# Performance work log

Hardware: AMD Instinct MI355X
Metric: run time of the kernel (lower is better)

Reference implementation:

```python
import jax, jax.numpy as jnp
from jax import lax
import numpy as np

DIM = 256
N_EMBED = 512
B = 16
T = 2048


def setup_inputs() -> dict:
    key = jax.random.key(0)
    k1, k2, k3 = jax.random.split(key, 3)
    inp = jax.random.normal(k1, (B, T, DIM), dtype=jnp.float32)
    spk = jax.random.normal(k2, (3, B, DIM), dtype=jnp.float32)
    embedding = jax.random.normal(k3, (N_EMBED, DIM, DIM), dtype=jnp.float32)
    return {"input": inp, "speaker_embedding": spk, "embedding": embedding}


def reference(input, speaker_embedding, embedding):
    x = input                              # (B, T, D)
    mul = speaker_embedding[2].T           # (D, B)
    add = speaker_embedding[1].T           # (D, B)
    # per-batch codebook: (n, D, D) @ (D, B) -> (n, D, B)
    cb = jnp.einsum('ndk,kb->ndb', embedding, mul)
    cb = cb / jnp.linalg.norm(cb, axis=1, keepdims=True)
    cb = cb + add                          # broadcast (D,B) over n
    embed = jnp.transpose(cb, (2, 1, 0))   # (B, D, n)
    # distances on detached values (matches torch .detach())
    flat = lax.stop_gradient(x)
    e = lax.stop_gradient(embed)
    dist = (jnp.sum(flat * flat, axis=2, keepdims=True)
            - 2.0 * jnp.einsum('btd,bdn->btn', flat, e)
            + jnp.sum(e * e, axis=1, keepdims=True))  # (B, T, n)
    embed_ind = jnp.argmax(-dist, axis=2)  # (B, T)
    cbB = jnp.transpose(cb, (2, 0, 1))     # (B, n, D)
    # per-batch gather of selected codes -> (B, T, D)
    quantize = cbB[jnp.arange(cbB.shape[0])[:, None], embed_ind]
    diff = jnp.mean((quantize - x) ** 2)
    quantize_1 = x + lax.stop_gradient(quantize - x)
    return ((quantize + quantize_1) / 2.0, diff, embed_ind)
```

## Files before the change

### kernel.cpp

```cpp
#include <hip/hip_runtime.h>

#define T_   2048
#define D_   256
#define N_   512
#define BTOT 16

typedef unsigned short ushortT;

#define QN   ((size_t)BTOT*T_*D_)
#define IDX0 (QN + 1)

__device__ __forceinline__ float bf2f(ushortT u){
    union { unsigned int i; float f; } c; c.i = ((unsigned int)u) << 16; return c.f;
}
__device__ __forceinline__ void unp8(uint4 p, float* f){
    f[0]=bf2f((ushortT)(p.x & 0xffff)); f[1]=bf2f((ushortT)(p.x >> 16));
    f[2]=bf2f((ushortT)(p.y & 0xffff)); f[3]=bf2f((ushortT)(p.y >> 16));
    f[4]=bf2f((ushortT)(p.z & 0xffff)); f[5]=bf2f((ushortT)(p.z >> 16));
    f[6]=bf2f((ushortT)(p.w & 0xffff)); f[7]=bf2f((ushortT)(p.w >> 16));
}
__device__ __forceinline__ void unp4(uint2 p, float* f){
    f[0]=bf2f((ushortT)(p.x & 0xffff)); f[1]=bf2f((ushortT)(p.x >> 16));
    f[2]=bf2f((ushortT)(p.y & 0xffff)); f[3]=bf2f((ushortT)(p.y >> 16));
}

__global__ void k_probe(const ushortT* __restrict__ x, int* __restrict__ flg){
    int tid = threadIdx.x;
    ushortT u = x[tid];
    int e = (u >> 7) & 0xff;
    bool ok = (e >= 100 && e <= 140);
    unsigned long long m = __ballot(ok);
    if (tid == 0) *flg = (__popcll(m) >= 55) ? 1 : 0;
}

template<int BC>
__global__ __launch_bounds__(256) void k_codebook(
    const void* __restrict__ spkin, const void* __restrict__ embin,
    float* __restrict__ cbw, int b0, const int* __restrict__ flagp)
{
    const int isb = *flagp;
    const ushortT* ss = (const ushortT*)spkin;
    const float*   sf = (const float*)spkin;
    const ushortT* es = (const ushortT*)embin;
    const float*   ef = (const float*)embin;

    __shared__ float s2[D_ * 16];
    __shared__ float s1[D_ * 16];
    __shared__ float red[16 * D_];
    __shared__ float nrm[16];

    const int n = blockIdx.x, tid = threadIdx.x;

    for (int e = tid; e < D_ * 16; e += 256){ s2[e] = 0.f; s1[e] = 0.f; }
    __syncthreads();
    for (int e = tid; e < D_ * BC; e += 256){
        int bl = e >> 8, k = e & 255;
        int g2 = (2*BTOT + b0 + bl)*D_ + k;
        int g1 = (1*BTOT + b0 + bl)*D_ + k;
        s2[k*16 + bl] = isb ? bf2f(ss[g2]) : sf[g2];
        s1[k*16 + bl] = isb ? bf2f(ss[g1]) : sf[g1];
    }
    __syncthreads();

    const int d = tid;
    float acc[16];
    #pragma unroll
    for (int b = 0; b < 16; b++) acc[b] = 0.f;

    const size_t rb = ((size_t)n * D_ + d) * D_;

    auto inner = [&](const float* ev, int k0){
        #pragma unroll
        for (int j = 0; j < 8; j++){
            float e = ev[j];
            if (BC == 16){
                const float4* sp = (const float4*)&s2[(k0 + j) * 16];
                float4 q0 = sp[0], q1 = sp[1], q2 = sp[2], q3 = sp[3];
                acc[0]  += e*q0.x; acc[1]  += e*q0.y; acc[2]  += e*q0.z; acc[3]  += e*q0.w;
                acc[4]  += e*q1.x; acc[5]  += e*q1.y; acc[6]  += e*q1.z; acc[7]  += e*q1.w;
                acc[8]  += e*q2.x; acc[9]  += e*q2.y; acc[10] += e*q2.z; acc[11] += e*q2.w;
                acc[12] += e*q3.x; acc[13] += e*q3.y; acc[14] += e*q3.z; acc[15] += e*q3.w;
            } else {
                #pragma unroll
                for (int bl = 0; bl < BC; bl++)
                    acc[bl] += e * s2[(k0 + j)*16 + bl];
            }
        }
    };

    if (isb){
        for (int k0 = 0; k0 < D_; k0 += 8){
            uint4 p = *(const uint4*)(es + rb + k0);
            float ev[8]; unp8(p, ev);
            inner(ev, k0);
        }
    } else {
        for (int k0 = 0; k0 < D_; k0 += 8){
            float4 p0 = *(const float4*)(ef + rb + k0);
            float4 p1 = *(const float4*)(ef + rb + k0 + 4);
            float ev[8] = {p0.x,p0.y,p0.z,p0.w,p1.x,p1.y,p1.z,p1.w};
            inner(ev, k0);
        }
    }

    #pragma unroll
    for (int bl = 0; bl < BC; bl++) red[bl*D_ + d] = acc[bl]*acc[bl];
    __syncthreads();
    for (int s = 128; s > 0; s >>= 1){
        if (d < s){
            #pragma unroll
            for (int bl = 0; bl < BC; bl++) red[bl*D_ + d] += red[bl*D_ + d + s];
        }
        __syncthreads();
    }
    if (d < BC) nrm[d] = sqrtf(red[d*D_]);
    __syncthreads();

    #pragma unroll
    for (int bl = 0; bl < BC; bl++){
        float cb = acc[bl] / nrm[bl] + s1[d*16 + bl];
        cbw[((size_t)bl*N_ + n)*D_ + d] = cb;
    }
}

__global__ __launch_bounds__(512, 2) void k_gemm(
    const void* __restrict__ xin, const float* __restrict__ cbw,
    float* __restrict__ outf, int blk0, const int* __restrict__ flagp)
{
    const int isb = *flagp;
    const int bl = blockIdx.x >> 4, tT = blockIdx.x & 15;
    const int bg = blk0 + bl;

    __shared__ float As[16 * 132];
    __shared__ float Bs[16 * 256];
    __shared__ float e2p[512];

    const int tid = threadIdx.x;
    const int tx = tid & 31, ty = tid >> 5;
    const int rA = tid >> 2, qA = tid & 3;
    const int rB = tid >> 1, hB = tid & 1;

    const float*   xf = (const float*)xin;
    const ushortT* xs = (const ushortT*)xin;
    const size_t xbase = ((size_t)bg*T_ + tT*128 + rA)*D_ + qA*4;

    float runv[8]; int runi[8];
    #pragma unroll
    for (int i = 0; i < 8; i++){ runv[i] = 3.4e38f; runi[i] = 0x7fffffff; }

    for (int nT = 0; nT < 2; nT++){
        float acc[8][8];
        #pragma unroll
        for (int i = 0; i < 8; i++)
            #pragma unroll
            for (int j = 0; j < 8; j++) acc[i][j] = 0.f;
        float e2acc = 0.f;

        const size_t bbase = ((size_t)bl*N_ + nT*256 + rB)*D_ + hB*8;

        for (int k0 = 0; k0 < D_; k0 += 16){
            float av[4];
            if (isb){
                uint2 p = *(const uint2*)(xs + xbase + k0);
                unp4(p, av);
            } else {
                float4 p = *(const float4*)(xf + xbase + k0);
                av[0]=p.x; av[1]=p.y; av[2]=p.z; av[3]=p.w;
            }
            float bv[8];
            {
                float4 q0 = *(const float4*)(cbw + bbase + k0);
                float4 q1 = *(const float4*)(cbw + bbase + k0 + 4);
                bv[0]=q0.x; bv[1]=q0.y; bv[2]=q0.z; bv[3]=q0.w;
                bv[4]=q1.x; bv[5]=q1.y; bv[6]=q1.z; bv[7]=q1.w;
            }
            #pragma unroll
            for (int j = 0; j < 8; j++) e2acc += bv[j]*bv[j];

            #pragma unroll
            for (int j = 0; j < 4; j++) As[(qA*4 + j)*132 + rA] = av[j];
            #pragma unroll
            for (int j = 0; j < 8; j++) Bs[(hB*8 + j)*256 + rB] = bv[j];
            __syncthreads();

            #pragma unroll
            for (int kl = 0; kl < 16; kl++){
                float4 a0 = *(const float4*)&As[kl*132 + (ty<<2)];
                float4 a1 = *(const float4*)&As[kl*132 + 64 + (ty<<2)];
                float4 c0 = *(const float4*)&Bs[kl*256 + (tx<<2)];
                float4 c1 = *(const float4*)&Bs[kl*256 + 128 + (tx<<2)];
                float ar[8] = {a0.x,a0.y,a0.z,a0.w,a1.x,a1.y,a1.z,a1.w};
                float br[8] = {c0.x,c0.y,c0.z,c0.w,c1.x,c1.y,c1.z,c1.w};
                #pragma unroll
                for (int i = 0; i < 8; i++)
                    #pragma unroll
                    for (int j = 0; j < 8; j++)
                        acc[i][j] += ar[i]*br[j];
            }
            __syncthreads();
        }

        e2p[rB*2 + hB] = e2acc;
        __syncthreads();

        float e2c[8];
        #pragma unroll
        for (int j = 0; j < 8; j++){
            int nl = (tx<<2) + (j&3) + ((j>>2)<<7);
            e2c[j] = e2p[nl*2] + e2p[nl*2 + 1];
        }

        #pragma unroll
        for (int i = 0; i < 8; i++){
            #pragma unroll
            for (int j = 0; j < 8; j++){
                int ng = nT*256 + (tx<<2) + (j&3) + ((j>>2)<<7);
                float s = e2c[j] - 2.f*acc[i][j];
                if (s < runv[i] || (s == runv[i] && ng < runi[i])){
                    runv[i] = s; runi[i] = ng;
                }
            }
        }
    }

    #pragma unroll
    for (int m = 16; m >= 1; m >>= 1){
        #pragma unroll
        for (int i = 0; i < 8; i++){
            float ov = __shfl_xor(runv[i], m);
            int   on = __shfl_xor(runi[i], m);
            if (ov < runv[i] || (ov == runv[i] && on < runi[i])){
                runv[i] = ov; runi[i] = on;
            }
        }
    }
    if (tx == 0){
        #pragma unroll
        for (int i = 0; i < 8; i++){
            int row = (ty<<2) + (i&3) + ((i>>2)<<6);
            outf[IDX0 + (size_t)bg*T_ + tT*128 + row] = (float)runi[i];
        }
    }
}

__global__ __launch_bounds__(256) void k_gather(
    const void* __restrict__ xin, const float* __restrict__ cbw,
    float* __restrict__ outf, float* __restrict__ part,
    int blk0, const int* __restrict__ flagp)
{
    const int isb = *flagp;
    const int bid = blockIdx.x;
    const int bl = bid >> 11, t = bid & 2047;
    const int bg = blk0 + bl;
    const int tid = threadIdx.x;

    const int n = (int)outf[IDX0 + (size_t)bg*T_ + t];

    const float*   xf = (const float*)xin;
    const ushortT* xs = (const ushortT*)xin;
    const size_t rowbase = ((size_t)bg*T_ + t)*D_;
    float xv = isb ? bf2f(xs[rowbase + tid]) : xf[rowbase + tid];
    float q  = cbw[((size_t)bl*N_ + n)*D_ + tid];
    float qm = q - xv;
    float q1 = xv + qm;
    outf[rowbase + tid] = 0.5f*(q + q1);

    float val = qm*qm;
    #pragma unroll
    for (int o = 32; o > 0; o >>= 1) val += __shfl_down(val, o, 64);
    __shared__ float wsum[4];
    if ((tid & 63) == 0) wsum[tid >> 6] = val;
    __syncthreads();
    if (tid == 0)
        atomicAdd(&part[bid & 1023], wsum[0] + wsum[1] + wsum[2] + wsum[3]);
}

__global__ __launch_bounds__(256) void k_fin(const float* __restrict__ part,
                                             float* __restrict__ outf){
    const int tid = threadIdx.x;
    float v = part[tid] + part[tid + 256] + part[tid + 512] + part[tid + 768];
    #pragma unroll
    for (int o = 32; o > 0; o >>= 1) v += __shfl_down(v, o, 64);
    __shared__ float wsum[4];
    if ((tid & 63) == 0) wsum[tid >> 6] = v;
    __syncthreads();
    if (tid == 0)
        outf[QN] = (wsum[0] + wsum[1] + wsum[2] + wsum[3]) * (1.0f / (float)QN);
}

extern "C" void kernel_launch(void* const* d_in, const int* in_sizes, int n_in,
                              void* d_out, int out_size, void* d_ws, size_t ws_size,
                              hipStream_t stream)
{
    const void* x   = d_in[0];
    const void* spk = d_in[1];
    const void* emb = d_in[2];

    int Bc = 16;
    while (Bc > 1 && ((size_t)Bc*N_*D_*4 + 4096 + 16) > ws_size) Bc >>= 1;

    char*  ws   = (char*)d_ws;
    float* cbw  = (float*)ws;
    size_t tail = (size_t)Bc*N_*D_*4;
    float* part = (float*)(ws + tail);
    int*   flg  = (int*)  (ws + tail + 4096);

    float* outf = (float*)d_out;

    hipMemsetAsync(part, 0, 4096, stream);
    k_probe<<<1, 64, 0, stream>>>((const ushortT*)x, flg);

    for (int b0 = 0; b0 < BTOT; b0 += Bc){
        switch (Bc){
            case 16: k_codebook<16><<<512, 256, 0, stream>>>(spk, emb, cbw, b0, flg); break;
            case 8:  k_codebook<8> <<<512, 256, 0, stream>>>(spk, emb, cbw, b0, flg); break;
            case 4:  k_codebook<4> <<<512, 256, 0, stream>>>(spk, emb, cbw, b0, flg); break;
            case 2:  k_codebook<2> <<<512, 256, 0, stream>>>(spk, emb, cbw, b0, flg); break;
            default: k_codebook<1> <<<512, 256, 0, stream>>>(spk, emb, cbw, b0, flg); break;
        }
        k_gemm  <<<Bc*16,   512, 0, stream>>>(x, cbw, outf, b0, flg);
        k_gather<<<Bc*2048, 256, 0, stream>>>(x, cbw, outf, part, b0, flg);
    }
    k_fin<<<1, 256, 0, stream>>>(part, outf);
}
```

Baseline: 384.3 us.

## Fuse gather into distance GEMM, widen N tile to full codebook, prefetch loads

The GEMM kernel now covers all 512 codes in one pass, with a 16-wide accumulator per thread, instead of two 256-code passes. This avoids reloading the x tile twice. Global loads for the next k-slice are issued before the inner FMA loop as a register prefetch. The separate gather kernel is folded into the GEMM epilogue: the block's selected indices go to shared memory and the block then writes the quantized rows and accumulates the squared error with vectorized loads. The larger accumulator (128 floats per thread) and doubled shared-memory B tile raise register pressure and may lower occupancy under launch_bounds(512,2).

```diff
diff --git a/kernel.cpp b/kernel.cpp
--- a/kernel.cpp
+++ b/kernel.cpp
@@ -125,104 +125,108 @@
 
 __global__ __launch_bounds__(512, 2) void k_gemm(
     const void* __restrict__ xin, const float* __restrict__ cbw,
-    float* __restrict__ outf, int blk0, const int* __restrict__ flagp)
+    float* __restrict__ outf, float* __restrict__ part,
+    int blk0, const int* __restrict__ flagp)
 {
     const int isb = *flagp;
     const int bl = blockIdx.x >> 4, tT = blockIdx.x & 15;
     const int bg = blk0 + bl;
 
     __shared__ float As[16 * 132];
-    __shared__ float Bs[16 * 256];
-    __shared__ float e2p[512];
+    __shared__ float Bs[16 * 512];
+    __shared__ float e2p[1024];
+    __shared__ int   sidx[128];
+    __shared__ float wred[8];
 
     const int tid = threadIdx.x;
     const int tx = tid & 31, ty = tid >> 5;
     const int rA = tid >> 2, qA = tid & 3;
-    const int rB = tid >> 1, hB = tid & 1;
 
     const float*   xf = (const float*)xin;
     const ushortT* xs = (const ushortT*)xin;
     const size_t xbase = ((size_t)bg*T_ + tT*128 + rA)*D_ + qA*4;
+    const size_t bbase = ((size_t)bl*N_ + tid)*D_;
+
+    float acc[8][16];
+    #pragma unroll
+    for (int i = 0; i < 8; i++)
+        #pragma unroll
+        for (int j = 0; j < 16; j++) acc[i][j] = 0.f;
+    float e2lo = 0.f, e2hi = 0.f;
+
+    float av[4], bv[16];
+    {
+        if (isb){ uint2 p = *(const uint2*)(xs + xbase); unp4(p, av); }
+        else    { float4 p = *(const float4*)(xf + xbase);
+                  av[0]=p.x; av[1]=p.y; av[2]=p.z; av[3]=p.w; }
+        #pragma unroll
+        for (int q = 0; q < 4; q++){
+            float4 c = *(const float4*)(cbw + bbase + q*4);
+            bv[q*4+0]=c.x; bv[q*4+1]=c.y; bv[q*4+2]=c.z; bv[q*4+3]=c.w;
+        }
+    }
+
+    for (int k0 = 0; k0 < D_; k0 += 16){
+        #pragma unroll
+        for (int j = 0; j < 4; j++) As[(qA*4 + j)*132 + rA] = av[j];
+        #pragma unroll
+        for (int k = 0; k < 16; k++) Bs[k*512 + tid] = bv[k];
+        #pragma unroll
+        for (int k = 0; k < 8; k++)  e2lo += bv[k]*bv[k];
+        #pragma unroll
+        for (int k = 8; k < 16; k++) e2hi += bv[k]*bv[k];
+        __syncthreads();
+
+        if (k0 + 16 < D_){
+            if (isb){ uint2 p = *(const uint2*)(xs + xbase + k0 + 16); unp4(p, av); }
+            else    { float4 p = *(const float4*)(xf + xbase + k0 + 16);
+                      av[0]=p.x; av[1]=p.y; av[2]=p.z; av[3]=p.w; }
+            #pragma unroll
+            for (int q = 0; q < 4; q++){
+                float4 c = *(const float4*)(cbw + bbase + k0 + 16 + q*4);
+                bv[q*4+0]=c.x; bv[q*4+1]=c.y; bv[q*4+2]=c.z; bv[q*4+3]=c.w;
+            }
+        }
+
+        #pragma unroll
+        for (int kl = 0; kl < 16; kl++){
+            float4 a0 = *(const float4*)&As[kl*132 + (ty<<2)];
+            float4 a1 = *(const float4*)&As[kl*132 + 64 + (ty<<2)];
+            float4 c0 = *(const float4*)&Bs[kl*512 + (tx<<2)];
+            float4 c1 = *(const float4*)&Bs[kl*512 + 128 + (tx<<2)];
+            float4 c2 = *(const float4*)&Bs[kl*512 + 256 + (tx<<2)];
+            float4 c3 = *(const float4*)&Bs[kl*512 + 384 + (tx<<2)];
+            float ar[8]  = {a0.x,a0.y,a0.z,a0.w,a1.x,a1.y,a1.z,a1.w};
+            float br[16] = {c0.x,c0.y,c0.z,c0.w,c1.x,c1.y,c1.z,c1.w,
+                            c2.x,c2.y,c2.z,c2.w,c3.x,c3.y,c3.z,c3.w};
+            #pragma unroll
+            for (int i = 0; i < 8; i++)
+                #pragma unroll
+                for (int j = 0; j < 16; j++)
+                    acc[i][j] += ar[i]*br[j];
+        }
+        __syncthreads();
+    }
+
+    e2p[tid*2]     = e2lo;
+    e2p[tid*2 + 1] = e2hi;
+    __syncthreads();
 
     float runv[8]; int runi[8];
     #pragma unroll
     for (int i = 0; i < 8; i++){ runv[i] = 3.4e38f; runi[i] = 0x7fffffff; }
-
-    for (int nT = 0; nT < 2; nT++){
-        float acc[8][8];
-        #pragma unroll
-        for (int i = 0; i < 8; i++)
-            #pragma unroll
-            for (int j = 0; j < 8; j++) acc[i][j] = 0.f;
-        float e2acc = 0.f;
-
-        const size_t bbase = ((size_t)bl*N_ + nT*256 + rB)*D_ + hB*8;
-
-        for (int k0 = 0; k0 < D_; k0 += 16){
-            float av[4];
-            if (isb){
-                uint2 p = *(const uint2*)(xs + xbase + k0);
-                unp4(p, av);
-            } else {
-                float4 p = *(const float4*)(xf + xbase + k0);
-                av[0]=p.x; av[1]=p.y; av[2]=p.z; av[3]=p.w;
+    #pragma unroll
+    for (int j = 0; j < 16; j++){
+        int col = ((j>>2)<<7) + (tx<<2) + (j&3);
+        float e2c = e2p[col*2] + e2p[col*2 + 1];
+        #pragma unroll
+        for (int i = 0; i < 8; i++){
+            float s = e2c - 2.f*acc[i][j];
+            if (s < runv[i] || (s == runv[i] && col < runi[i])){
+                runv[i] = s; runi[i] = col;
             }
-            float bv[8];
-            {
-                float4 q0 = *(const float4*)(cbw + bbase + k0);
-                float4 q1 = *(const float4*)(cbw + bbase + k0 + 4);
-                bv[0]=q0.x; bv[1]=q0.y; bv[2]=q0.z; bv[3]=q0.w;
-                bv[4]=q1.x; bv[5]=q1.y; bv[6]=q1.z; bv[7]=q1.w;
-            }
-            #pragma unroll
-            for (int j = 0; j < 8; j++) e2acc += bv[j]*bv[j];
-
-            #pragma unroll
-            for (int j = 0; j < 4; j++) As[(qA*4 + j)*132 + rA] = av[j];
-            #pragma unroll
-            for (int j = 0; j < 8; j++) Bs[(hB*8 + j)*256 + rB] = bv[j];
-            __syncthreads();
-
-            #pragma unroll
-            for (int kl = 0; kl < 16; kl++){
-                float4 a0 = *(const float4*)&As[kl*132 + (ty<<2)];
-                float4 a1 = *(const float4*)&As[kl*132 + 64 + (ty<<2)];
-                float4 c0 = *(const float4*)&Bs[kl*256 + (tx<<2)];
-                float4 c1 = *(const float4*)&Bs[kl*256 + 128 + (tx<<2)];
-                float ar[8] = {a0.x,a0.y,a0.z,a0.w,a1.x,a1.y,a1.z,a1.w};
-                float br[8] = {c0.x,c0.y,c0.z,c0.w,c1.x,c1.y,c1.z,c1.w};
-                #pragma unroll
-                for (int i = 0; i < 8; i++)
-                    #pragma unroll
-                    for (int j = 0; j < 8; j++)
-                        acc[i][j] += ar[i]*br[j];
-            }
-            __syncthreads();
-        }
-
-        e2p[rB*2 + hB] = e2acc;
-        __syncthreads();
-
-        float e2c[8];
-        #pragma unroll
-        for (int j = 0; j < 8; j++){
-            int nl = (tx<<2) + (j&3) + ((j>>2)<<7);
-            e2c[j] = e2p[nl*2] + e2p[nl*2 + 1];
-        }
-
-        #pragma unroll
-        for (int i = 0; i < 8; i++){
-            #pragma unroll
-            for (int j = 0; j < 8; j++){
-                int ng = nT*256 + (tx<<2) + (j&3) + ((j>>2)<<7);
-                float s = e2c[j] - 2.f*acc[i][j];
-                if (s < runv[i] || (s == runv[i] && ng < runi[i])){
-                    runv[i] = s; runi[i] = ng;
-                }
-            }
-        }
-    }
-
+        }
+    }
     #pragma unroll
     for (int m = 16; m >= 1; m >>= 1){
         #pragma unroll
@@ -238,41 +242,44 @@
         #pragma unroll
         for (int i = 0; i < 8; i++){
             int row = (ty<<2) + (i&3) + ((i>>2)<<6);
+            sidx[row] = runi[i];
             outf[IDX0 + (size_t)bg*T_ + tT*128 + row] = (float)runi[i];
         }
     }
-}
-
-__global__ __launch_bounds__(256) void k_gather(
-    const void* __restrict__ xin, const float* __restrict__ cbw,
-    float* __restrict__ outf, float* __restrict__ part,
-    int blk0, const int* __restrict__ flagp)
-{
-    const int isb = *flagp;
-    const int bid = blockIdx.x;
-    const int bl = bid >> 11, t = bid & 2047;
-    const int bg = blk0 + bl;
-    const int tid = threadIdx.x;
-
-    const int n = (int)outf[IDX0 + (size_t)bg*T_ + t];
-
-    const float*   xf = (const float*)xin;
-    const ushortT* xs = (const ushortT*)xin;
-    const size_t rowbase = ((size_t)bg*T_ + t)*D_;
-    float xv = isb ? bf2f(xs[rowbase + tid]) : xf[rowbase + tid];
-    float q  = cbw[((size_t)bl*N_ + n)*D_ + tid];
-    float qm = q - xv;
-    float q1 = xv + qm;
-    outf[rowbase + tid] = 0.5f*(q + q1);
-
-    float val = qm*qm;
-    #pragma unroll
-    for (int o = 32; o > 0; o >>= 1) val += __shfl_down(val, o, 64);
-    __shared__ float wsum[4];
-    if ((tid & 63) == 0) wsum[tid >> 6] = val;
-    __syncthreads();
-    if (tid == 0)
-        atomicAdd(&part[bid & 1023], wsum[0] + wsum[1] + wsum[2] + wsum[3]);
+    __syncthreads();
+
+    const int d4 = (tid & 63) << 2;
+    const int rg = tid >> 6;
+    float dacc = 0.f;
+    #pragma unroll 4
+    for (int it = 0; it < 16; it++){
+        int r = it*8 + rg;
+        int n = sidx[r];
+        size_t xrow = ((size_t)bg*T_ + tT*128 + r)*D_ + d4;
+        float xv[4];
+        if (isb){ uint2 p = *(const uint2*)(xs + xrow); unp4(p, xv); }
+        else    { float4 p = *(const float4*)(xf + xrow);
+                  xv[0]=p.x; xv[1]=p.y; xv[2]=p.z; xv[3]=p.w; }
+        float4 q = *(const float4*)(cbw + ((size_t)bl*N_ + n)*D_ + d4);
+        float m0 = q.x - xv[0], m1 = q.y - xv[1], m2 = q.z - xv[2], m3 = q.w - xv[3];
+        float4 o;
+        o.x = 0.5f*(q.x + (xv[0] + m0));
+        o.y = 0.5f*(q.y + (xv[1] + m1));
+        o.z = 0.5f*(q.z + (xv[2] + m2));
+        o.w = 0.5f*(q.w + (xv[3] + m3));
+        *(float4*)(outf + xrow) = o;
+        dacc += m0*m0 + m1*m1 + m2*m2 + m3*m3;
+    }
+    #pragma unroll
+    for (int o = 32; o > 0; o >>= 1) dacc += __shfl_down(dacc, o, 64);
+    if ((tid & 63) == 0) wred[tid >> 6] = dacc;
+    __syncthreads();
+    if (tid == 0){
+        float s = 0.f;
+        #pragma unroll
+        for (int w = 0; w < 8; w++) s += wred[w];
+        atomicAdd(&part[blockIdx.x & 1023], s);
+    }
 }
 
 __global__ __launch_bounds__(256) void k_fin(const float* __restrict__ part,
@@ -318,8 +325,7 @@
             case 2:  k_codebook<2> <<<512, 256, 0, stream>>>(spk, emb, cbw, b0, flg); break;
             default: k_codebook<1> <<<512, 256, 0, stream>>>(spk, emb, cbw, b0, flg); break;
         }
-        k_gemm  <<<Bc*16,   512, 0, stream>>>(x, cbw, outf, b0, flg);
-        k_gather<<<Bc*2048, 256, 0, stream>>>(x, cbw, outf, part, b0, flg);
+        k_gemm<<<Bc*16, 512, 0, stream>>>(x, cbw, outf, part, b0, flg);
     }
     k_fin<<<1, 256, 0, stream>>>(part, outf);
 }
```

Result: slower. 631.0 us (+64.2%).
